# Kernel tuning notes

Measured on AMD Instinct MI355X. Metric: run time of the kernel, lower is better.

## Reference

```python
import jax, jax.numpy as jnp
import numpy as np


def setup_inputs() -> dict:
    key = jax.random.key(0)
    k1, k2, k3 = jax.random.split(key, 3)
    B, S, A, C = 128, 52, 5, 20
    predictions = jax.random.normal(k1, (B, A * (5 + C), S, S), dtype=jnp.float32)
    t = jax.random.uniform(k2, (B, S, S, A, 5 + C), dtype=jnp.float32)
    mask = (jax.random.uniform(k3, (B, S, S, A)) < 0.05).astype(jnp.float32)
    targets = t.at[..., 4].set(mask)
    anchors = jnp.array([[1.08, 1.19], [3.42, 4.41], [6.63, 11.38],
                         [9.42, 5.11], [16.62, 10.52]], dtype=jnp.float32)
    return {"predictions": predictions, "targets": targets, "anchors": anchors}


def _yolov2_loss(predictions, targets, anchors):
    B, pred_dim, S, _ = predictions.shape
    A = anchors.shape[0]
    C = pred_dim // A - 5
    # [B, A, 5+C, S, S] -> [B, S, S, A, 5+C]
    p = predictions.reshape(B, A, 5 + C, S, S).transpose(0, 3, 4, 1, 2)
    tx, ty, tw, th = p[..., 0], p[..., 1], p[..., 2], p[..., 3]
    conf_logits = p[..., 4]
    class_logits = p[..., 5:]

    gx, gy, gw, gh = targets[..., 0], targets[..., 1], targets[..., 2], targets[..., 3]
    obj_mask = targets[..., 4]
    class_target = targets[..., 5:]

    pred_cx = jax.nn.sigmoid(tx)
    pred_cy = jax.nn.sigmoid(ty)
    pred_w = jnp.exp(tw) * anchors[:, 0]  # broadcast over trailing A dim
    pred_h = jnp.exp(th) * anchors[:, 1]

    # grid offsets: dim 1 is i (row -> cy), dim 2 is j (col -> cx)
    jj = jnp.arange(S, dtype=jnp.float32)[None, None, :, None]
    ii = jnp.arange(S, dtype=jnp.float32)[None, :, None, None]
    cx_gt, cy_gt = gx + jj, gy + ii
    cx_pr, cy_pr = pred_cx + jj, pred_cy + ii

    # vectorized corner-form IoU (only used where obj_mask == 1)
    x1min, x1max = cx_gt - gw / 2, cx_gt + gw / 2
    y1min, y1max = cy_gt - gh / 2, cy_gt + gh / 2
    x2min, x2max = cx_pr - pred_w / 2, cx_pr + pred_w / 2
    y2min, y2max = cy_pr - pred_h / 2, cy_pr + pred_h / 2
    inter_w = jnp.clip(jnp.minimum(x1max, x2max) - jnp.maximum(x1min, x2min), 0.0)
    inter_h = jnp.clip(jnp.minimum(y1max, y2max) - jnp.maximum(y1min, y2min), 0.0)
    inter = inter_w * inter_h
    union = gw * gh + pred_w * pred_h - inter
    iou = jnp.where(union > 0, inter / union, 0.0)

    loss_xy = jnp.sum(obj_mask * (jnp.square(pred_cx - gx) + jnp.square(pred_cy - gy)))
    eps = 1e-6
    loss_wh = jnp.sum(obj_mask * (jnp.square(jnp.sqrt(pred_w + eps) - jnp.sqrt(gw + eps))
                                  + jnp.square(jnp.sqrt(pred_h + eps) - jnp.sqrt(gh + eps))))

    conf_pred = jax.nn.sigmoid(conf_logits)
    loss_obj = jnp.sum(obj_mask * jnp.square(iou - conf_pred))
    loss_noobj = jnp.sum((1.0 - obj_mask) * jnp.square(conf_pred))

    # BCE with logits: softplus(x) - x * t (stable via logaddexp)
    bce = jnp.logaddexp(0.0, class_logits) - class_logits * class_target
    loss_cls = jnp.sum(obj_mask[..., None] * bce)

    total = 5.0 * (loss_xy + loss_wh) + 5.0 * loss_obj + 0.5 * loss_noobj + loss_cls
    return total, loss_xy + loss_wh, loss_cls, loss_obj + loss_noobj


def reference(predictions, targets, anchors):
    # returns (total, coord, class, obj) matching the original dict values
    return _yolov2_loss(predictions, targets, anchors)
```

## Files before the change

### kernel.cpp

```cpp
#include <hip/hip_runtime.h>

#define SS 2704
#define NA 5
#define NC 20
#define NB 128
#define CELLS (NB * SS)
#define TILE 64
#define TPB 320
#define NBLK (CELLS / TILE)
#define RBLOCK 1024

__device__ __forceinline__ float fast_sigmoid(float x) {
    return __builtin_amdgcn_rcpf(1.0f + __expf(-x));
}
__device__ __forceinline__ float fast_softplus(float x) {
    return fmaxf(x, 0.0f) + __logf(1.0f + __expf(-fabsf(x)));
}

__global__ __launch_bounds__(TPB) void yolo_main(
        const float* __restrict__ P,
        const float* __restrict__ T,
        const float* __restrict__ anch,
        float* __restrict__ partial) {
    __shared__ float red[NA][4];

    int a    = threadIdx.x >> 6;
    int lane = threadIdx.x & 63;
    int base_cell = blockIdx.x * TILE;
    int cell = base_cell + lane;
    int b    = cell / SS;
    int ij   = cell - b * SS;
    int b0   = base_cell / SS;
    int ij0  = base_cell - b0 * SS;

    const float* Ta = T + (size_t)cell * 125 + a * 25;
    const float* Pa = P + ((size_t)b * 125 + a * 25) * SS + ij;
    float aw  = anch[2 * a];
    float ahv = anch[2 * a + 1];

    float fl = Ta[4];
    float cp = fast_sigmoid(Pa[4 * SS]);

    float s_xywh = 0.0f, s_cls = 0.0f, s_obj = 0.0f, s_noobj = 0.0f;
    bool isobj = (fl != 0.0f);

    if (isobj) {
        float tx = Pa[0], ty = Pa[SS], tw = Pa[2 * SS], th = Pa[3 * SS];
        float gx = Ta[0], gy = Ta[1], gw = Ta[2], gh = Ta[3];
        float cx = fast_sigmoid(tx), cy = fast_sigmoid(ty);
        float pw = __expf(tw) * aw;
        float ph = __expf(th) * ahv;
        float iw = fmaxf(fminf(gx + 0.5f * gw, cx + 0.5f * pw) -
                         fmaxf(gx - 0.5f * gw, cx - 0.5f * pw), 0.0f);
        float ih = fmaxf(fminf(gy + 0.5f * gh, cy + 0.5f * ph) -
                         fmaxf(gy - 0.5f * gh, cy - 0.5f * ph), 0.0f);
        float inter = iw * ih;
        float uni   = gw * gh + pw * ph - inter;
        float iou   = (uni > 0.0f) ? inter * __builtin_amdgcn_rcpf(uni) : 0.0f;

        float dx = cx - gx, dy = cy - gy;
        s_xywh += dx * dx + dy * dy;
        const float eps = 1e-6f;
        float dw = __fsqrt_rn(pw + eps) - __fsqrt_rn(gw + eps);
        float dh = __fsqrt_rn(ph + eps) - __fsqrt_rn(gh + eps);
        s_xywh += dw * dw + dh * dh;

        float dob = iou - cp;
        s_obj += dob * dob;
    } else {
        s_noobj = cp * cp;
    }

    unsigned long long act = __ballot(isobj);
    int nact = __popcll(act);
    int slot_off = lane / 20;
    int c = lane - slot_off * 20;
    unsigned long long m = act;
    for (int basep = 0; basep < nact; basep += 3) {
        unsigned long long m0 = m;
        unsigned long long m1 = m0 & (m0 - 1);
        unsigned long long m2 = m1 & (m1 - 1);
        int src0 = __ffsll(m0) - 1;
        int src1 = __ffsll(m1) - 1;
        int src2 = __ffsll(m2) - 1;
        m = m2 & (m2 - 1);

        int s   = basep + slot_off;
        int src = (slot_off == 0) ? src0 : (slot_off == 1) ? src1 : src2;
        if (slot_off < 3 && s < nact) {
            int pij = ij0 + src;
            int pb  = b0;
            if (pij >= SS) { pij -= SS; pb += 1; }
            int pcell = base_cell + src;
            float t = T[(size_t)pcell * 125 + a * 25 + 5 + c];
            float l = P[((size_t)pb * 125 + a * 25 + 5 + c) * SS + pij];
            s_cls += fast_softplus(l) - l * t;
        }
    }

    #pragma unroll
    for (int off = 32; off > 0; off >>= 1) {
        s_xywh  += __shfl_xor(s_xywh,  off, 64);
        s_cls   += __shfl_xor(s_cls,   off, 64);
        s_obj   += __shfl_xor(s_obj,   off, 64);
        s_noobj += __shfl_xor(s_noobj, off, 64);
    }
    if (lane == 0) {
        red[a][0] = s_xywh; red[a][1] = s_cls; red[a][2] = s_obj; red[a][3] = s_noobj;
    }
    __syncthreads();
    if (threadIdx.x == 0) {
        float r0 = 0, r1 = 0, r2 = 0, r3 = 0;
        #pragma unroll
        for (int w = 0; w < NA; ++w) {
            r0 += red[w][0]; r1 += red[w][1]; r2 += red[w][2]; r3 += red[w][3];
        }
        float* p = partial + (size_t)blockIdx.x * 4;
        p[0] = r0; p[1] = r1; p[2] = r2; p[3] = r3;
    }
}

__global__ __launch_bounds__(RBLOCK) void yolo_reduce(
        const float* __restrict__ partial, int n, float* __restrict__ out) {
    float v0 = 0.0f, v1 = 0.0f, v2 = 0.0f, v3 = 0.0f;
    for (int i = threadIdx.x; i < n; i += RBLOCK) {
        const float* p = partial + (size_t)i * 4;
        v0 += p[0]; v1 += p[1]; v2 += p[2]; v3 += p[3];
    }
    #pragma unroll
    for (int off = 32; off > 0; off >>= 1) {
        v0 += __shfl_xor(v0, off, 64);
        v1 += __shfl_xor(v1, off, 64);
        v2 += __shfl_xor(v2, off, 64);
        v3 += __shfl_xor(v3, off, 64);
    }
    __shared__ float red[RBLOCK / 64][4];
    int wid = threadIdx.x >> 6, lane = threadIdx.x & 63;
    if (lane == 0) {
        red[wid][0] = v0; red[wid][1] = v1; red[wid][2] = v2; red[wid][3] = v3;
    }
    __syncthreads();
    if (threadIdx.x == 0) {
        float xywh = 0, cls = 0, obj = 0, noobj = 0;
        #pragma unroll
        for (int q = 0; q < RBLOCK / 64; ++q) {
            xywh += red[q][0]; cls += red[q][1]; obj += red[q][2]; noobj += red[q][3];
        }
        out[0] = 5.0f * xywh + 5.0f * obj + 0.5f * noobj + cls;
        out[1] = xywh;
        out[2] = cls;
        out[3] = obj + noobj;
    }
}

extern "C" void kernel_launch(void* const* d_in, const int* in_sizes, int n_in,
                              void* d_out, int out_size, void* d_ws, size_t ws_size,
                              hipStream_t stream) {
    const float* P = (const float*)d_in[0];
    const float* T = (const float*)d_in[1];
    const float* anch = (const float*)d_in[2];
    float* out = (float*)d_out;
    float* partial = (float*)d_ws;

    yolo_main<<<NBLK, TPB, 0, stream>>>(P, T, anch, partial);
    yolo_reduce<<<1, RBLOCK, 0, stream>>>(partial, NBLK, out);
}
```

Baseline: 57.38 us.

## Precompute objectness mask with a separate streaming pass over targets

Adds a pre-pass kernel that reads the whole targets tensor with coalesced float4 loads and writes a compact byte mask of objectness flags. The main kernel then reads this mask instead of the strided per-cell objectness float. The aim is to avoid the scattered 100-byte-strided loads in the main kernel. The cost is that the pre-pass streams all of T (about 173 MB), far more than the sparse reads it replaces, and it adds an extra launch.

After: 80.85 us. +40.9%, slower.

```diff
diff --git a/kernel.cpp b/kernel.cpp
--- a/kernel.cpp
+++ b/kernel.cpp
@@ -9,6 +9,11 @@
 #define TPB 320
 #define NBLK (CELLS / TILE)
 #define RBLOCK 1024
+#define T_DWORDS (CELLS * 125)
+#define T_F4 (T_DWORDS / 4)
+#define MASK_BYTES ((size_t)CELLS * NA)
+#define FLAG_TPB 256
+#define FLAG_BLOCKS 2048
 
 __device__ __forceinline__ float fast_sigmoid(float x) {
     return __builtin_amdgcn_rcpf(1.0f + __expf(-x));
@@ -17,10 +22,34 @@
     return fmaxf(x, 0.0f) + __logf(1.0f + __expf(-fabsf(x)));
 }
 
+__global__ __launch_bounds__(FLAG_TPB) void yolo_flags(
+        const float4* __restrict__ T4, unsigned char* __restrict__ mask) {
+    const int stride = FLAG_TPB * FLAG_BLOCKS;
+    for (int i = blockIdx.x * FLAG_TPB + threadIdx.x; i < T_F4; i += stride) {
+        float4 v = T4[i];
+        int g0   = i * 4;
+        int cell = g0 / 125;
+        int r    = g0 - cell * 125;
+        float vc0 = v.x, vc1 = v.y, vc2 = v.z, vc3 = v.w;
+        #pragma unroll
+        for (int c = 0; c < 4; ++c) {
+            float vv = (c == 0) ? vc0 : (c == 1) ? vc1 : (c == 2) ? vc2 : vc3;
+            int rr = r + c;
+            int cc = cell;
+            if (rr >= 125) { rr -= 125; cc += 1; }
+            int q = rr / 25;
+            if (rr - q * 25 == 4)
+                mask[(size_t)cc * NA + q] = (vv != 0.0f) ? 1 : 0;
+        }
+    }
+}
+
+template <bool USE_MASK>
 __global__ __launch_bounds__(TPB) void yolo_main(
         const float* __restrict__ P,
         const float* __restrict__ T,
         const float* __restrict__ anch,
+        const unsigned char* __restrict__ mask,
         float* __restrict__ partial) {
     __shared__ float red[NA][4];
 
@@ -30,19 +59,20 @@
     int cell = base_cell + lane;
     int b    = cell / SS;
     int ij   = cell - b * SS;
-    int b0   = base_cell / SS;
-    int ij0  = base_cell - b0 * SS;
 
     const float* Ta = T + (size_t)cell * 125 + a * 25;
     const float* Pa = P + ((size_t)b * 125 + a * 25) * SS + ij;
     float aw  = anch[2 * a];
     float ahv = anch[2 * a + 1];
 
-    float fl = Ta[4];
+    bool isobj;
+    if (USE_MASK)
+        isobj = mask[(size_t)cell * NA + a] != 0;
+    else
+        isobj = (Ta[4] != 0.0f);
     float cp = fast_sigmoid(Pa[4 * SS]);
 
     float s_xywh = 0.0f, s_cls = 0.0f, s_obj = 0.0f, s_noobj = 0.0f;
-    bool isobj = (fl != 0.0f);
 
     if (isobj) {
         float tx = Pa[0], ty = Pa[SS], tw = Pa[2 * SS], th = Pa[3 * SS];
@@ -88,13 +118,12 @@
         int s   = basep + slot_off;
         int src = (slot_off == 0) ? src0 : (slot_off == 1) ? src1 : src2;
         if (slot_off < 3 && s < nact) {
-            int pij = ij0 + src;
-            int pb  = b0;
-            if (pij >= SS) { pij -= SS; pb += 1; }
             int pcell = base_cell + src;
-            float t = T[(size_t)pcell * 125 + a * 25 + 5 + c];
-            float l = P[((size_t)pb * 125 + a * 25 + 5 + c) * SS + pij];
-            s_cls += fast_softplus(l) - l * t;
+            int pb    = pcell / SS;
+            int pij   = pcell - pb * SS;
+            float tt = T[(size_t)pcell * 125 + a * 25 + 5 + c];
+            float l  = P[((size_t)pb * 125 + a * 25 + 5 + c) * SS + pij];
+            s_cls += fast_softplus(l) - l * tt;
         }
     }
 
@@ -160,8 +189,17 @@
     const float* T = (const float*)d_in[1];
     const float* anch = (const float*)d_in[2];
     float* out = (float*)d_out;
-    float* partial = (float*)d_ws;
-
-    yolo_main<<<NBLK, TPB, 0, stream>>>(P, T, anch, partial);
-    yolo_reduce<<<1, RBLOCK, 0, stream>>>(partial, NBLK, out);
-}
+
+    size_t need = MASK_BYTES + (size_t)NBLK * 4 * sizeof(float);
+    if (ws_size >= need) {
+        unsigned char* mask = (unsigned char*)d_ws;
+        float* partial = (float*)((char*)d_ws + MASK_BYTES);
+        yolo_flags<<<FLAG_BLOCKS, FLAG_TPB, 0, stream>>>((const float4*)T, mask);
+        yolo_main<true><<<NBLK, TPB, 0, stream>>>(P, T, anch, mask, partial);
+        yolo_reduce<<<1, RBLOCK, 0, stream>>>(partial, NBLK, out);
+    } else {
+        float* partial = (float*)d_ws;
+        yolo_main<false><<<NBLK, TPB, 0, stream>>>(P, T, anch, nullptr, partial);
+        yolo_reduce<<<1, RBLOCK, 0, stream>>>(partial, NBLK, out);
+    }
+}
```
